# Performance work log

Measured on AMD Instinct MI355X. Metric: run time of the kernel, lower is better.

## Reference

```python
import jax, jax.numpy as jnp
import numpy as np

GROUPS = 4
KLD_SCALE = 10.0
COMMITMENT_COST = 0.25


def setup_inputs() -> dict:
    key = jax.random.key(0)
    k1, k2 = jax.random.split(key)
    z = jax.random.normal(k1, (8, 4096, 512), dtype=jnp.float32)
    embed_w = jax.random.normal(k2, (512, 128), dtype=jnp.float32)
    return {"z": z, "embed_w": embed_w}


def reference(z, embed_w):
    B, N, D = z.shape
    d = D // GROUPS  # sub-vector dim per group
    flat = z.reshape(B * N * GROUPS, d)  # [M, d]
    # squared euclidean distance to each codebook entry: [M, K]
    dist = (
        jnp.sum(flat * flat, axis=1, keepdims=True)
        - 2.0 * flat @ embed_w.T
        + jnp.sum(embed_w * embed_w, axis=1)[None, :]
    )
    ind = jnp.argmin(dist, axis=1)  # argmax(-dist)
    z_q = embed_w[ind]  # [M, d] codebook gather
    sg = jax.lax.stop_gradient
    diff = KLD_SCALE * (
        COMMITMENT_COST * jnp.mean((sg(z_q) - flat) ** 2)
        + jnp.mean((z_q - sg(flat)) ** 2)
    )
    # straight-through estimator
    z_q_st = (flat + sg(z_q - flat)).reshape(B, N, D)
    ind_out = ind.reshape(N, B, GROUPS)  # matches torch .view on contiguous buffer
    return (z_q_st, diff, ind_out)
```

## Files before the change

### kernel.cpp

```cpp
#include <hip/hip_runtime.h>
#include <float.h>


typedef _Float16 half8 __attribute__((ext_vector_type(8)));
typedef __attribute__((ext_vector_type(4))) float f32x4;

constexpr int Dn = 128;
constexpr int K  = 512;
constexpr long long Mrows = 131072;
constexpr int RPW   = 32;
constexpr int WAVES = 16;
constexpr int RPB   = RPW * WAVES;
constexpr int NBLK  = (int)(Mrows / RPB);
constexpr float TAU_A = 0.05f;

constexpr size_t ZQ_SIZE  = (size_t)Mrows * Dn;
constexpr size_t DIFF_OFF = ZQ_SIZE;
constexpr size_t IND_OFF  = ZQ_SIZE + 1;

__device__ inline void gload_lds16(const void* g, void* l) {
    __builtin_amdgcn_global_load_lds(
        (const __attribute__((address_space(1))) unsigned int*)g,
        (__attribute__((address_space(3))) unsigned int*)l,
        16, 0, 0);
}

__global__ void wnorm_kernel(const float* __restrict__ W, float* __restrict__ wn2) {
    int k = blockIdx.x * blockDim.x + threadIdx.x;
    if (k < K) {
        double s = 0.0;
        const float* w = W + (size_t)k * Dn;
        #pragma unroll 4
        for (int i = 0; i < Dn; ++i) { double v = (double)w[i]; s += v * v; }
        wn2[k] = (float)(-0.5 * s);
    }
}

__global__ void prep_kernel(const float* __restrict__ W, unsigned short* __restrict__ Wp) {
    int t = blockIdx.x * 256 + threadIdx.x;
    int code = t >> 4;
    int gs   = t & 15;
    int g    = gs ^ (code & 7);
    const float* src = W + (size_t)code * Dn + g * 8;
    ushort4 h[2];
    #pragma unroll
    for (int half = 0; half < 2; ++half) {
        float4 v = *(const float4*)(src + half * 4);
        float vv[4] = {v.x, v.y, v.z, v.w};
        unsigned short* hp = (unsigned short*)&h[half];
        #pragma unroll
        for (int e = 0; e < 4; ++e) {
            _Float16 hh = (_Float16)vv[e];
            hp[e] = __builtin_bit_cast(unsigned short, hh);
        }
    }
    size_t base = (size_t)t * 8;
    *(ushort4*)(Wp + base)     = h[0];
    *(ushort4*)(Wp + base + 4) = h[1];
}

__global__ __launch_bounds__(1024, 4) void vq_main(
        const float* __restrict__ Z, const float* __restrict__ W,
        const unsigned short* __restrict__ Wp, const float* __restrict__ wn2,
        float* __restrict__ out, double* __restrict__ diffsum) {
    __shared__ __align__(16) char Wlds[131072];
    __shared__ float wn2_s[K];
    __shared__ float xn_s[RPB];
    __shared__ int   sIdx[RPB];
    __shared__ int   flagList[RPB];
    __shared__ int   flagN;
    __shared__ float wpart[WAVES];

    const int tid  = threadIdx.x;
    const int w    = tid >> 6;
    const int lane = tid & 63;
    const int lm   = lane & 15;
    const int lg   = lane >> 4;
    const size_t row0 = (size_t)blockIdx.x * RPB;

    if (tid == 0) flagN = 0;

    {
        const char* gsrc = (const char*)Wp;
        #pragma unroll
        for (int it = 0; it < 8; ++it) {
            const int gbase = it * 1024 + w * 64;
            gload_lds16(gsrc + (size_t)(gbase + lane) * 16, Wlds + (size_t)gbase * 16);
        }
    }
    if (tid < K) wn2_s[tid] = wn2[tid];

    half8 ah[2][4];
    #pragma unroll
    for (int r = 0; r < 2; ++r) {
        const size_t grow = row0 + (size_t)w * RPW + r * 16 + lm;
        float s2 = 0.f;
        #pragma unroll
        for (int ks = 0; ks < 4; ++ks) {
            const float* xp = Z + grow * Dn + ks * 32 + lg * 8;
            float4 x0 = *(const float4*)xp;
            float4 x1 = *(const float4*)(xp + 4);
            float xv[8] = {x0.x, x0.y, x0.z, x0.w, x1.x, x1.y, x1.z, x1.w};
            #pragma unroll
            for (int j = 0; j < 8; ++j) {
                ah[r][ks][j] = (_Float16)xv[j];
                s2 += xv[j] * xv[j];
            }
        }
        s2 += __shfl_xor(s2, 16);
        s2 += __shfl_xor(s2, 32);
        if (lg == 0) xn_s[w * RPW + r * 16 + lm] = s2;
    }

    float m1[2][4], m2[2][4];
    int   i1[2][4];
    #pragma unroll
    for (int r = 0; r < 2; ++r)
        #pragma unroll
        for (int j = 0; j < 4; ++j) { m1[r][j] = -FLT_MAX; m2[r][j] = -FLT_MAX; i1[r][j] = 0; }

    asm volatile("s_waitcnt vmcnt(0)" ::: "memory");
    __syncthreads();

    #pragma unroll 2
    for (int t = 0; t < 32; ++t) {
        const int code = t * 16 + lm;
        const float cinit = wn2_s[code];
        half8 bh[4];
        #pragma unroll
        for (int ks = 0; ks < 4; ++ks) {
            const int off = code * 256 + ((((ks << 2) + lg) ^ (code & 7)) << 4);
            bh[ks] = *(const half8*)(Wlds + off);
        }
        f32x4 acc[2];
        #pragma unroll
        for (int r = 0; r < 2; ++r) acc[r] = (f32x4){cinit, cinit, cinit, cinit};
        #pragma unroll
        for (int ks = 0; ks < 4; ++ks) {
            #pragma unroll
            for (int r = 0; r < 2; ++r)
                acc[r] = __builtin_amdgcn_mfma_f32_16x16x32_f16(ah[r][ks], bh[ks], acc[r], 0, 0, 0);
        }
        #pragma unroll
        for (int r = 0; r < 2; ++r) {
            #pragma unroll
            for (int j = 0; j < 4; ++j) {
                const float a = acc[r][j];
                m2[r][j] = __builtin_amdgcn_fmed3f(a, m1[r][j], m2[r][j]);
                const bool gt = a > m1[r][j];
                m1[r][j] = fmaxf(m1[r][j], a);
                i1[r][j] = gt ? code : i1[r][j];
            }
        }
    }

    #pragma unroll
    for (int sft = 1; sft < 16; sft <<= 1) {
        #pragma unroll
        for (int r = 0; r < 2; ++r) {
            #pragma unroll
            for (int j = 0; j < 4; ++j) {
                float o1 = __shfl_xor(m1[r][j], sft);
                float o2 = __shfl_xor(m2[r][j], sft);
                int   oi = __shfl_xor(i1[r][j], sft);
                if (o1 > m1[r][j] || (o1 == m1[r][j] && oi < i1[r][j])) {
                    m2[r][j] = fmaxf(m1[r][j], o2);
                    m1[r][j] = o1;
                    i1[r][j] = oi;
                } else {
                    m2[r][j] = fmaxf(m2[r][j], o1);
                }
            }
        }
    }

    float psum = 0.f;
    if (lm == 0) {
        #pragma unroll
        for (int r = 0; r < 2; ++r) {
            #pragma unroll
            for (int j = 0; j < 4; ++j) {
                const int row = w * RPW + r * 16 + lg * 4 + j;
                sIdx[row] = i1[r][j];
                psum += xn_s[row] - 2.f * m1[r][j];
                if (m1[r][j] - m2[r][j] < TAU_A) {
                    int pos = atomicAdd(&flagN, 1);
                    flagList[pos] = row;
                }
            }
        }
    }
    __syncthreads();

    {
        const int nflag = flagN;
        const int cg    = lane >> 3;
        const int dbase = (lane & 7) * 16;
        for (int fi = w; fi < nflag; fi += WAVES) {
            const int rr = flagList[fi];
            const float* xp = Z + (row0 + rr) * Dn + dbase;
            double xd[16];
            #pragma unroll
            for (int q = 0; q < 16; q += 4) {
                float4 v = *(const float4*)(xp + q);
                xd[q] = v.x; xd[q+1] = v.y; xd[q+2] = v.z; xd[q+3] = v.w;
            }
            double best = 1e300; int bi = 0;
            for (int cb = 0; cb < 64; ++cb) {
                const int c = cb * 8 + cg;
                const float* wp = W + (size_t)c * Dn + dbase;
                double s = 0.0;
                #pragma unroll
                for (int q = 0; q < 16; q += 4) {
                    float4 wv = *(const float4*)(wp + q);
                    double d0 = xd[q]   - (double)wv.x;
                    double d1 = xd[q+1] - (double)wv.y;
                    double d2 = xd[q+2] - (double)wv.z;
                    double d3 = xd[q+3] - (double)wv.w;
                    s += d0 * d0 + d1 * d1 + d2 * d2 + d3 * d3;
                }
                s += __shfl_xor(s, 1);
                s += __shfl_xor(s, 2);
                s += __shfl_xor(s, 4);
                if (s < best) { best = s; bi = c; }
            }
            #pragma unroll
            for (int sft = 8; sft < 64; sft <<= 1) {
                double ob = __shfl_xor(best, sft);
                int    ok = __shfl_xor(bi, sft);
                if (ob < best || (ob == best && ok < bi)) { best = ob; bi = ok; }
            }
            if (lane == 0) sIdx[rr] = bi;
        }
    }
    __syncthreads();

    #pragma unroll
    for (int it = 0; it < 16; ++it) {
        int f4i = tid + it * 1024;
        int row = f4i >> 5, cq = f4i & 31;
        int ind = sIdx[row];
        float4 wv = ((const float4*)(W + (size_t)ind * Dn))[cq];
        ((float4*)(out + (row0 + row) * Dn))[cq] = wv;
    }
    if (tid < RPB) out[IND_OFF + row0 + tid] = (float)sIdx[tid];

    #pragma unroll
    for (int sft = 1; sft < 64; sft <<= 1) psum += __shfl_xor(psum, sft);
    if (lane == 0) wpart[w] = psum;
    __syncthreads();
    if (tid == 0) {
        double t = 0.0;
        #pragma unroll
        for (int i = 0; i < WAVES; ++i) t += (double)wpart[i];
        atomicAdd(diffsum, t);
    }
}

__global__ void diff_kernel(const double* __restrict__ diffsum, float* __restrict__ out) {
    if (threadIdx.x == 0 && blockIdx.x == 0) {
        out[DIFF_OFF] = (float)(12.5 * diffsum[0] / (double)ZQ_SIZE);
    }
}

extern "C" void kernel_launch(void* const* d_in, const int* in_sizes, int n_in,
                              void* d_out, int out_size, void* d_ws, size_t ws_size,
                              hipStream_t stream) {
    (void)in_sizes; (void)n_in; (void)out_size; (void)ws_size;
    const float* Z = (const float*)d_in[0];
    const float* W = (const float*)d_in[1];
    float* out = (float*)d_out;
    double* diffsum = (double*)d_ws;
    float* wn2 = (float*)((char*)d_ws + 16);
    unsigned short* Wp = (unsigned short*)((char*)d_ws + 4096);

    hipMemsetAsync(d_ws, 0, 16, stream);
    wnorm_kernel<<<2, 256, 0, stream>>>(W, wn2);
    prep_kernel<<<32, 256, 0, stream>>>(W, Wp);
    vq_main<<<NBLK, 1024, 0, stream>>>(Z, W, Wp, wn2, out, diffsum);
    diff_kernel<<<1, 64, 0, stream>>>(diffsum, out);
}
```

Baseline: 112.9 us.

## Fuse codebook norm into prep kernel, stagger tile order, per-wave gather

Merges the codebook-norm kernel into the fp16 prep kernel using a shuffle reduction, which removes one launch and also emits double-precision norms. Each wave now starts the code-tile loop at a different offset, to spread LDS bank access across waves. The fp64 refinement of near-tie rows switches from squared differences to a dot product plus a precomputed norm, roughly halving its arithmetic. The output gather is reorganised so each wave writes its own rows, which may help locality but changes the store pattern.

```diff
diff --git a/kernel.cpp b/kernel.cpp
--- a/kernel.cpp
+++ b/kernel.cpp
@@ -25,43 +25,39 @@
         16, 0, 0);
 }
 
-__global__ void wnorm_kernel(const float* __restrict__ W, float* __restrict__ wn2) {
-    int k = blockIdx.x * blockDim.x + threadIdx.x;
-    if (k < K) {
-        double s = 0.0;
-        const float* w = W + (size_t)k * Dn;
-        #pragma unroll 4
-        for (int i = 0; i < Dn; ++i) { double v = (double)w[i]; s += v * v; }
-        wn2[k] = (float)(-0.5 * s);
-    }
-}
-
-__global__ void prep_kernel(const float* __restrict__ W, unsigned short* __restrict__ Wp) {
+__global__ void prep_kernel(const float* __restrict__ W,
+                            unsigned short* __restrict__ Wp,
+                            float* __restrict__ wn2,
+                            double* __restrict__ wn64) {
     int t = blockIdx.x * 256 + threadIdx.x;
     int code = t >> 4;
-    int gs   = t & 15;
-    int g    = gs ^ (code & 7);
+    int g    = t & 15;
     const float* src = W + (size_t)code * Dn + g * 8;
-    ushort4 h[2];
-    #pragma unroll
-    for (int half = 0; half < 2; ++half) {
-        float4 v = *(const float4*)(src + half * 4);
-        float vv[4] = {v.x, v.y, v.z, v.w};
-        unsigned short* hp = (unsigned short*)&h[half];
-        #pragma unroll
-        for (int e = 0; e < 4; ++e) {
-            _Float16 hh = (_Float16)vv[e];
-            hp[e] = __builtin_bit_cast(unsigned short, hh);
-        }
-    }
-    size_t base = (size_t)t * 8;
-    *(ushort4*)(Wp + base)     = h[0];
-    *(ushort4*)(Wp + base + 4) = h[1];
+    float4 a = *(const float4*)src;
+    float4 b = *(const float4*)(src + 4);
+    float vv[8] = {a.x, a.y, a.z, a.w, b.x, b.y, b.z, b.w};
+    half8 hv;
+    double s2 = 0.0;
+    #pragma unroll
+    for (int j = 0; j < 8; ++j) {
+        hv[j] = (_Float16)vv[j];
+        s2 += (double)vv[j] * (double)vv[j];
+    }
+    *(half8*)((char*)Wp + (size_t)code * 256 + ((g ^ (code & 7)) << 4)) = hv;
+    s2 += __shfl_xor(s2, 1);
+    s2 += __shfl_xor(s2, 2);
+    s2 += __shfl_xor(s2, 4);
+    s2 += __shfl_xor(s2, 8);
+    if (g == 0) {
+        wn2[code]  = (float)(-0.5 * s2);
+        wn64[code] = s2;
+    }
 }
 
 __global__ __launch_bounds__(1024, 4) void vq_main(
         const float* __restrict__ Z, const float* __restrict__ W,
         const unsigned short* __restrict__ Wp, const float* __restrict__ wn2,
+        const double* __restrict__ wn64,
         float* __restrict__ out, double* __restrict__ diffsum) {
     __shared__ __align__(16) char Wlds[131072];
     __shared__ float wn2_s[K];
@@ -122,8 +118,10 @@
     asm volatile("s_waitcnt vmcnt(0)" ::: "memory");
     __syncthreads();
 
+    const int t0 = (w * 2) & 31;
     #pragma unroll 2
-    for (int t = 0; t < 32; ++t) {
+    for (int ti = 0; ti < 32; ++ti) {
+        const int t = (ti + t0) & 31;
         const int code = t * 16 + lm;
         const float cinit = wn2_s[code];
         half8 bh[4];
@@ -193,10 +191,10 @@
     __syncthreads();
 
     {
-        const int nflag = flagN;
+        const int nf = flagN;
         const int cg    = lane >> 3;
         const int dbase = (lane & 7) * 16;
-        for (int fi = w; fi < nflag; fi += WAVES) {
+        for (int fi = w; fi < nf; fi += WAVES) {
             const int rr = flagList[fi];
             const float* xp = Z + (row0 + rr) * Dn + dbase;
             double xd[16];
@@ -213,16 +211,16 @@
                 #pragma unroll
                 for (int q = 0; q < 16; q += 4) {
                     float4 wv = *(const float4*)(wp + q);
-                    double d0 = xd[q]   - (double)wv.x;
-                    double d1 = xd[q+1] - (double)wv.y;
-                    double d2 = xd[q+2] - (double)wv.z;
-                    double d3 = xd[q+3] - (double)wv.w;
-                    s += d0 * d0 + d1 * d1 + d2 * d2 + d3 * d3;
+                    s += xd[q]   * (double)wv.x;
+                    s += xd[q+1] * (double)wv.y;
+                    s += xd[q+2] * (double)wv.z;
+                    s += xd[q+3] * (double)wv.w;
                 }
                 s += __shfl_xor(s, 1);
                 s += __shfl_xor(s, 2);
                 s += __shfl_xor(s, 4);
-                if (s < best) { best = s; bi = c; }
+                const double sc = wn64[c] - 2.0 * s;
+                if (sc < best) { best = sc; bi = c; }
             }
             #pragma unroll
             for (int sft = 8; sft < 64; sft <<= 1) {
@@ -237,13 +235,14 @@
 
     #pragma unroll
     for (int it = 0; it < 16; ++it) {
-        int f4i = tid + it * 1024;
-        int row = f4i >> 5, cq = f4i & 31;
-        int ind = sIdx[row];
+        int f4i = lane + it * 64;
+        int rl  = f4i >> 5, cq = f4i & 31;
+        int ind = sIdx[w * RPW + rl];
         float4 wv = ((const float4*)(W + (size_t)ind * Dn))[cq];
-        ((float4*)(out + (row0 + row) * Dn))[cq] = wv;
-    }
-    if (tid < RPB) out[IND_OFF + row0 + tid] = (float)sIdx[tid];
+        ((float4*)(out + (row0 + w * RPW + rl) * Dn))[cq] = wv;
+    }
+    if (lane < RPW)
+        out[IND_OFF + row0 + w * RPW + lane] = (float)sIdx[w * RPW + lane];
 
     #pragma unroll
     for (int sft = 1; sft < 64; sft <<= 1) psum += __shfl_xor(psum, sft);
@@ -271,12 +270,12 @@
     const float* W = (const float*)d_in[1];
     float* out = (float*)d_out;
     double* diffsum = (double*)d_ws;
-    float* wn2 = (float*)((char*)d_ws + 16);
-    unsigned short* Wp = (unsigned short*)((char*)d_ws + 4096);
+    float*  wn2  = (float*)((char*)d_ws + 64);
+    double* wn64 = (double*)((char*)d_ws + 2112);
+    unsigned short* Wp = (unsigned short*)((char*)d_ws + 8192);
 
     hipMemsetAsync(d_ws, 0, 16, stream);
-    wnorm_kernel<<<2, 256, 0, stream>>>(W, wn2);
-    prep_kernel<<<32, 256, 0, stream>>>(W, Wp);
-    vq_main<<<NBLK, 1024, 0, stream>>>(Z, W, Wp, wn2, out, diffsum);
+    prep_kernel<<<32, 256, 0, stream>>>(W, Wp, wn2, wn64);
+    vq_main<<<NBLK, 1024, 0, stream>>>(Z, W, Wp, wn2, wn64, out, diffsum);
     diff_kernel<<<1, 64, 0, stream>>>(diffsum, out);
 }
```

After: 113.8 us. About the same (+0.8%).
